# Kernel optimization log

Measured on AMD Instinct MI355X. Metric: run time of the kernel, lower is better.

The kernel has to match this reference:

```python
import jax, jax.numpy as jnp
import numpy as np

N = 50000
E_RAND = 800000
F_IN = 256
F_OUT = 256
ALPHA = 0.2  # LeakyReLU negative slope


def setup_inputs() -> dict:
    key = jax.random.key(0)
    k1, k2, k3, k4 = jax.random.split(key, 4)
    x = jax.random.normal(k1, (N, F_IN), dtype=jnp.float32)
    # random edges + self-loops so every row has at least one edge (avoids div by 0)
    edge_rand = jax.random.randint(k2, (2, E_RAND), 0, N)
    loops = jnp.arange(N)
    edge = jnp.concatenate([edge_rand, jnp.stack([loops, loops])], axis=1)  # [2, 850000]
    W = jax.random.normal(k3, (F_IN, F_OUT), dtype=jnp.float32) * 0.05
    a = jax.random.normal(k4, (2 * F_OUT,), dtype=jnp.float32) * 0.05
    return {"x": x, "edge": edge, "W": W, "a": a}


def reference(x, edge, W, a):
    # x: [N, F_in], edge: [2, E] (row = dst/aggregation index per torch.sparse.mm(a, h))
    n = x.shape[0]
    f_out = W.shape[1]
    h = x @ W  # [N, F_out]
    src, dst = edge[0], edge[1]
    # a @ [h_src; h_dst] decomposes into two per-node dot products (no [E, 2F] concat)
    s = h @ a[:f_out]   # [N]
    t = h @ a[f_out:]   # [N]
    logit = s[src] + t[dst]                                  # [E]
    e = jnp.exp(-jax.nn.leaky_relu(logit, ALPHA))            # [E]
    rowsum = jax.ops.segment_sum(e, src, num_segments=n)     # [N]
    msg = e[:, None] * h[dst]                                # [E, F_out]
    h_prime = jax.ops.segment_sum(msg, src, num_segments=n)  # [N, F_out]
    h_prime = h_prime / rowsum[:, None]
    return jax.nn.relu(h_prime)  # concat=True path
```

## Files before the change

kernel.cpp:

```cpp
#include <hip/hip_runtime.h>
#include <hip/hip_fp16.h>

#define FDIM 256
#define ALPHA 0.2f

typedef _Float16 half8 __attribute__((ext_vector_type(8)));
typedef float floatx4 __attribute__((ext_vector_type(4)));

__global__ __launch_bounds__(256) void prep_hist(const float* __restrict__ W,
                                                 _Float16* __restrict__ wswz,
                                                 const int* __restrict__ edge,
                                                 int* __restrict__ deg, int E) {
  if (blockIdx.x < 32) {
    const int g = blockIdx.x * 256 + threadIdx.x;
    const int kc = g >> 11, L = g & 2047;
    const int n = L >> 3, c = L & 7;
    half8 hv;
#pragma unroll
    for (int j = 0; j < 8; ++j)
      hv[j] = (_Float16)W[(size_t)(kc * 64 + c * 8 + j) * 256 + n];
    *(half8*)(wswz + (size_t)g * 8) = hv;
  } else {
    const int e = (blockIdx.x - 32) * 256 + threadIdx.x;
    if (e < E) atomicAdd(&deg[edge[e]], 1);
  }
}

#define HT_STRIDE 264
__global__ __launch_bounds__(256) void gemm_mfma(
    const float* __restrict__ x, const _Float16* __restrict__ wswz,
    const float* __restrict__ a, _Float16* __restrict__ h,
    float* __restrict__ s, float* __restrict__ t, int M) {
  __shared__ __align__(16) _Float16 smem[64 * HT_STRIDE];
  _Float16* As = smem;
  const int tid = threadIdx.x;
  const int w = tid >> 6, l = tid & 63;
  const int l15 = l & 15, q = l >> 4;
  const int row0 = blockIdx.x * 64;

  floatx4 acc[4][4];
#pragma unroll
  for (int mt = 0; mt < 4; ++mt)
#pragma unroll
    for (int nt = 0; nt < 4; ++nt) acc[mt][nt] = (floatx4){0.f, 0.f, 0.f, 0.f};

  const int id0 = tid, id1 = 256 + tid;
  const int m0 = id0 >> 3, c0 = (id0 & 7) ^ (m0 & 7);
  const int m1 = id1 >> 3, c1 = (id1 & 7) ^ (m1 & 7);
  const int r0 = row0 + m0, r1 = row0 + m1;

  float4 pf[2][2];
  auto loadA = [&](int kc) {
    pf[0][0] = pf[0][1] = pf[1][0] = pf[1][1] = make_float4(0.f, 0.f, 0.f, 0.f);
    if (r0 < M) {
      const float4* p = (const float4*)(x + (size_t)r0 * 256 + kc * 64 + c0 * 8);
      pf[0][0] = p[0];
      pf[0][1] = p[1];
    }
    if (r1 < M) {
      const float4* p = (const float4*)(x + (size_t)r1 * 256 + kc * 64 + c1 * 8);
      pf[1][0] = p[0];
      pf[1][1] = p[1];
    }
  };
  auto storeA = [&]() {
#pragma unroll
    for (int hf = 0; hf < 2; ++hf) {
      half8 hv;
      hv[0] = (_Float16)pf[hf][0].x; hv[1] = (_Float16)pf[hf][0].y;
      hv[2] = (_Float16)pf[hf][0].z; hv[3] = (_Float16)pf[hf][0].w;
      hv[4] = (_Float16)pf[hf][1].x; hv[5] = (_Float16)pf[hf][1].y;
      hv[6] = (_Float16)pf[hf][1].z; hv[7] = (_Float16)pf[hf][1].w;
      *(half8*)(As + (size_t)(hf * 256 + tid) * 8) = hv;
    }
  };

  loadA(0);
  for (int kc = 0; kc < 4; ++kc) {
    storeA();
    half8 bf[2][4];
#pragma unroll
    for (int ks = 0; ks < 2; ++ks) {
      const int c = ks * 4 + q;
#pragma unroll
      for (int nt = 0; nt < 4; ++nt) {
        const int n = w * 64 + nt * 16 + l15;
        bf[ks][nt] = *(const half8*)(wswz + (size_t)(kc * 2048 + n * 8 + c) * 8);
      }
    }
    __syncthreads();
    if (kc < 3) loadA(kc + 1);
#pragma unroll
    for (int ks = 0; ks < 2; ++ks) {
      const int c = ks * 4 + q;
      half8 af[4];
#pragma unroll
      for (int mt = 0; mt < 4; ++mt) {
        const int m = mt * 16 + l15;
        af[mt] = *(const half8*)(As + (size_t)(m * 8 + (c ^ (m & 7))) * 8);
      }
#pragma unroll
      for (int mt = 0; mt < 4; ++mt)
#pragma unroll
        for (int nt = 0; nt < 4; ++nt)
          acc[mt][nt] = __builtin_amdgcn_mfma_f32_16x16x32_f16(
              af[mt], bf[ks][nt], acc[mt][nt], 0, 0, 0);
    }
    __syncthreads();
  }

#pragma unroll
  for (int mt = 0; mt < 4; ++mt)
#pragma unroll
    for (int nt = 0; nt < 4; ++nt)
#pragma unroll
      for (int r = 0; r < 4; ++r)
        smem[(size_t)(mt * 16 + q * 4 + r) * HT_STRIDE + w * 64 + nt * 16 +
             l15] = (_Float16)acc[mt][nt][r];
  __syncthreads();

  const int w8 = tid >> 5;
  const int colh = (tid & 31) * 8;
#pragma unroll
  for (int p = 0; p < 8; ++p) {
    const int rl = p * 8 + w8;
    const int row = row0 + rl;
    if (row < M)
      *(half8*)(h + (size_t)row * 256 + colh) =
          *(const half8*)(smem + (size_t)rl * HT_STRIDE + colh);
  }

  const int r8 = tid >> 2, seg = tid & 3;
  float sp = 0.f, tp = 0.f;
#pragma unroll
  for (int c8 = 0; c8 < 8; ++c8) {
    const int col = seg * 64 + c8 * 8;
    const half8 hv = *(const half8*)(smem + (size_t)r8 * HT_STRIDE + col);
    const float4 a0 = *(const float4*)(a + col);
    const float4 a1 = *(const float4*)(a + col + 4);
    const float4 b0 = *(const float4*)(a + 256 + col);
    const float4 b1 = *(const float4*)(a + 256 + col + 4);
    sp += (float)hv[0] * a0.x + (float)hv[1] * a0.y + (float)hv[2] * a0.z +
          (float)hv[3] * a0.w + (float)hv[4] * a1.x + (float)hv[5] * a1.y +
          (float)hv[6] * a1.z + (float)hv[7] * a1.w;
    tp += (float)hv[0] * b0.x + (float)hv[1] * b0.y + (float)hv[2] * b0.z +
          (float)hv[3] * b0.w + (float)hv[4] * b1.x + (float)hv[5] * b1.y +
          (float)hv[6] * b1.z + (float)hv[7] * b1.w;
  }
  sp += __shfl_xor(sp, 1);
  sp += __shfl_xor(sp, 2);
  tp += __shfl_xor(tp, 1);
  tp += __shfl_xor(tp, 2);
  if (seg == 0 && row0 + r8 < M) {
    s[row0 + r8] = sp;
    t[row0 + r8] = tp;
  }
}

__global__ __launch_bounds__(1024) void scan1(const int* __restrict__ deg,
                                              int* __restrict__ rowstart,
                                              int* __restrict__ bsum, int n) {
  const int tid = threadIdx.x;
  const int i = blockIdx.x * 1024 + tid;
  const int val = (i < n) ? deg[i] : 0;
  const int lane = tid & 63, wv = tid >> 6;
  int v = val;
#pragma unroll
  for (int off = 1; off < 64; off <<= 1) {
    const int o = __shfl_up(v, off);
    if (lane >= off) v += o;
  }
  __shared__ int wsum[16];
  __shared__ int woff[16];
  if (lane == 63) wsum[wv] = v;
  __syncthreads();
  if (tid < 16) {
    int wv2 = wsum[tid];
#pragma unroll
    for (int off = 1; off < 16; off <<= 1) {
      const int o = __shfl_up(wv2, off);
      if (tid >= off) wv2 += o;
    }
    woff[tid] = wv2;
  }
  __syncthreads();
  const int incl = v + (wv ? woff[wv - 1] : 0);
  if (i < n) rowstart[i] = incl - val;
  if (tid == 1023) bsum[blockIdx.x] = woff[15];
}

__global__ __launch_bounds__(64) void scan2(const int* __restrict__ bsum,
                                            int* __restrict__ boff,
                                            int* __restrict__ rowstart, int nb,
                                            int n) {
  const int tid = threadIdx.x;
  int v = (tid < nb) ? bsum[tid] : 0;
#pragma unroll
  for (int off = 1; off < 64; off <<= 1) {
    const int o = __shfl_up(v, off);
    if (tid >= off) v += o;
  }
  if (tid < nb) boff[tid] = v;
  if (tid == nb - 1) rowstart[n] = v;
}

__global__ __launch_bounds__(1024) void scan3(int* __restrict__ rowstart,
                                              int* __restrict__ rsc,
                                              const int* __restrict__ boff,
                                              int n) {
  const int i = blockIdx.x * 1024 + threadIdx.x;
  if (i < n) {
    const int v = rowstart[i] + (blockIdx.x ? boff[blockIdx.x - 1] : 0);
    rowstart[i] = v;
    rsc[i] = v;
  }
}

__global__ void scatter_kernel(const int* __restrict__ edge,
                               int* __restrict__ rsc,
                               const float* __restrict__ s,
                               const float* __restrict__ t,
                               int2* __restrict__ sde, int E) {
  const int e = blockIdx.x * 256 + threadIdx.x;
  if (e < E) {
    const int src = edge[e];
    const int dst = edge[E + e];
    const float logit = s[src] + t[dst];
    const float lr = logit > 0.f ? logit : ALPHA * logit;
    const float ev = __expf(-lr);
    const int pos = atomicAdd(&rsc[src], 1);
    sde[pos] = make_int2(dst, __float_as_int(ev));
  }
}

__global__ __launch_bounds__(256) void agg_kernel(
    const _Float16* __restrict__ h, const int* __restrict__ rowstart,
    const int2* __restrict__ sde, float* __restrict__ out, int n) {
  const int w = threadIdx.x >> 6, l = threadIdx.x & 63;
  const int row = blockIdx.x * 4 + w;
  if (row >= n) return;
  const int start = rowstart[row], end = rowstart[row + 1];
  const int half = l >> 5;
  const int lh = l & 31;
  const size_t fo = (size_t)lh * 8;
  float acc[8] = {};
  float rs = 0.f;
  int j = start;
  for (; j + 8 <= end; j += 8) {
#pragma unroll
    for (int u = 0; u < 4; ++u) {
      const int2 p = sde[j + u * 2 + half];
      const half8 v = *(const half8*)(h + (size_t)p.x * 256 + fo);
      const float e = __int_as_float(p.y);
      rs += e;
#pragma unroll
      for (int k = 0; k < 8; ++k) acc[k] += e * (float)v[k];
    }
  }
  for (; j < end; j += 2) {
    const int idx = j + half;
    const bool valid = idx < end;
    const int2 p = valid ? sde[idx] : make_int2(0, 0);
    const half8 v = *(const half8*)(h + (size_t)p.x * 256 + fo);
    const float e = valid ? __int_as_float(p.y) : 0.f;
    rs += e;
#pragma unroll
    for (int k = 0; k < 8; ++k) acc[k] += e * (float)v[k];
  }
  rs += __shfl_xor(rs, 32);
#pragma unroll
  for (int k = 0; k < 8; ++k) acc[k] += __shfl_xor(acc[k], 32);
  const float inv = 1.f / rs;
  float4 o;
#pragma unroll
  for (int k = 0; k < 4; ++k) {
    const float vv = acc[half * 4 + k] * inv;
    (&o.x)[k] = vv > 0.f ? vv : 0.f;
  }
  *(float4*)(out + (size_t)row * 256 + lh * 8 + half * 4) = o;
}

extern "C" void kernel_launch(void* const* d_in, const int* in_sizes, int n_in,
                              void* d_out, int out_size, void* d_ws,
                              size_t ws_size, hipStream_t stream) {
  const float* x = (const float*)d_in[0];
  const int* edge = (const int*)d_in[1];
  const float* W = (const float*)d_in[2];
  const float* a = (const float*)d_in[3];
  float* out = (float*)d_out;
  const int N = in_sizes[0] / FDIM;
  const int E = in_sizes[1] / 2;
  const int NB = (N + 1023) / 1024;

  _Float16* h = (_Float16*)d_ws;
  _Float16* wswz = h + (size_t)N * FDIM;
  float* s = (float*)(wswz + 8192 * 8);
  float* t = s + N;
  int* deg = (int*)(t + N);
  int* rsc = deg + N;
  int* rowstart = rsc + N;
  int* bsum = rowstart + N + 2;
  int* boff = bsum + 64;
  int2* sde = (int2*)(boff + 64);

  hipMemsetAsync(deg, 0, (size_t)N * sizeof(int), stream);

  prep_hist<<<32 + (E + 255) / 256, 256, 0, stream>>>(W, wswz, edge, deg, E);
  gemm_mfma<<<(N + 63) / 64, 256, 0, stream>>>(x, wswz, a, h, s, t, N);
  scan1<<<NB, 1024, 0, stream>>>(deg, rowstart, bsum, N);
  scan2<<<1, 64, 0, stream>>>(bsum, boff, rowstart, NB, N);
  scan3<<<NB, 1024, 0, stream>>>(rowstart, rsc, boff, N);
  scatter_kernel<<<(E + 255) / 256, 256, 0, stream>>>(edge, rsc, s, t, sde, E);
  agg_kernel<<<(N + 3) / 4, 256, 0, stream>>>(h, rowstart, sde, out, N);
}
```

Baseline: 272.2 us.

## Fuse scan into single-pass decoupled scan and move edge weight compute into aggregation

Result: slower. 328.0 us (+20.5%).

```diff
diff --git a/kernel.cpp b/kernel.cpp
--- a/kernel.cpp
+++ b/kernel.cpp
@@ -157,11 +157,14 @@
   }
 }
 
-__global__ __launch_bounds__(1024) void scan1(const int* __restrict__ deg,
-                                              int* __restrict__ rowstart,
-                                              int* __restrict__ bsum, int n) {
+__global__ __launch_bounds__(1024) void scan_one(const int* __restrict__ deg,
+                                                 int* __restrict__ rowstart,
+                                                 int* __restrict__ rsc,
+                                                 int* __restrict__ flags,
+                                                 int n, int nb) {
   const int tid = threadIdx.x;
-  const int i = blockIdx.x * 1024 + tid;
+  const int b = blockIdx.x;
+  const int i = b * 1024 + tid;
   const int val = (i < n) ? deg[i] : 0;
   const int lane = tid & 63, wv = tid >> 6;
   int v = val;
@@ -172,6 +175,7 @@
   }
   __shared__ int wsum[16];
   __shared__ int woff[16];
+  __shared__ int sbase;
   if (lane == 63) wsum[wv] = v;
   __syncthreads();
   if (tid < 16) {
@@ -185,61 +189,52 @@
   }
   __syncthreads();
   const int incl = v + (wv ? woff[wv - 1] : 0);
-  if (i < n) rowstart[i] = incl - val;
-  if (tid == 1023) bsum[blockIdx.x] = woff[15];
-}
-
-__global__ __launch_bounds__(64) void scan2(const int* __restrict__ bsum,
-                                            int* __restrict__ boff,
-                                            int* __restrict__ rowstart, int nb,
-                                            int n) {
-  const int tid = threadIdx.x;
-  int v = (tid < nb) ? bsum[tid] : 0;
-#pragma unroll
-  for (int off = 1; off < 64; off <<= 1) {
-    const int o = __shfl_up(v, off);
-    if (tid >= off) v += o;
-  }
-  if (tid < nb) boff[tid] = v;
-  if (tid == nb - 1) rowstart[n] = v;
-}
-
-__global__ __launch_bounds__(1024) void scan3(int* __restrict__ rowstart,
-                                              int* __restrict__ rsc,
-                                              const int* __restrict__ boff,
-                                              int n) {
-  const int i = blockIdx.x * 1024 + threadIdx.x;
+  const int aggregate = woff[15];
+  if (tid == 0) {
+    int base = 0;
+    if (b > 0) {
+      int f;
+      do {
+        f = __hip_atomic_load(&flags[b - 1], __ATOMIC_ACQUIRE,
+                              __HIP_MEMORY_SCOPE_AGENT);
+      } while (f == 0);
+      base = f - 1;
+    }
+    __hip_atomic_store(&flags[b], base + aggregate + 1, __ATOMIC_RELEASE,
+                       __HIP_MEMORY_SCOPE_AGENT);
+    sbase = base;
+  }
+  __syncthreads();
+  const int base = sbase;
   if (i < n) {
-    const int v = rowstart[i] + (blockIdx.x ? boff[blockIdx.x - 1] : 0);
-    rowstart[i] = v;
-    rsc[i] = v;
-  }
+    const int ex = base + incl - val;
+    rowstart[i] = ex;
+    rsc[i] = ex;
+  }
+  if (b == nb - 1 && tid == 0) rowstart[n] = base + aggregate;
 }
 
 __global__ void scatter_kernel(const int* __restrict__ edge,
-                               int* __restrict__ rsc,
-                               const float* __restrict__ s,
-                               const float* __restrict__ t,
-                               int2* __restrict__ sde, int E) {
+                               int* __restrict__ rsc, int* __restrict__ sdst,
+                               int E) {
   const int e = blockIdx.x * 256 + threadIdx.x;
   if (e < E) {
     const int src = edge[e];
     const int dst = edge[E + e];
-    const float logit = s[src] + t[dst];
-    const float lr = logit > 0.f ? logit : ALPHA * logit;
-    const float ev = __expf(-lr);
     const int pos = atomicAdd(&rsc[src], 1);
-    sde[pos] = make_int2(dst, __float_as_int(ev));
+    sdst[pos] = dst;
   }
 }
 
 __global__ __launch_bounds__(256) void agg_kernel(
-    const _Float16* __restrict__ h, const int* __restrict__ rowstart,
-    const int2* __restrict__ sde, float* __restrict__ out, int n) {
+    const _Float16* __restrict__ h, const float* __restrict__ s,
+    const float* __restrict__ t, const int* __restrict__ rowstart,
+    const int* __restrict__ sdst, float* __restrict__ out, int n) {
   const int w = threadIdx.x >> 6, l = threadIdx.x & 63;
   const int row = blockIdx.x * 4 + w;
   if (row >= n) return;
   const int start = rowstart[row], end = rowstart[row + 1];
+  const float srow = s[row];
   const int half = l >> 5;
   const int lh = l & 31;
   const size_t fo = (size_t)lh * 8;
@@ -249,9 +244,11 @@
   for (; j + 8 <= end; j += 8) {
 #pragma unroll
     for (int u = 0; u < 4; ++u) {
-      const int2 p = sde[j + u * 2 + half];
-      const half8 v = *(const half8*)(h + (size_t)p.x * 256 + fo);
-      const float e = __int_as_float(p.y);
+      const int d = sdst[j + u * 2 + half];
+      const float logit = srow + t[d];
+      const float lr = logit > 0.f ? logit : ALPHA * logit;
+      const float e = __expf(-lr);
+      const half8 v = *(const half8*)(h + (size_t)d * 256 + fo);
       rs += e;
 #pragma unroll
       for (int k = 0; k < 8; ++k) acc[k] += e * (float)v[k];
@@ -260,9 +257,11 @@
   for (; j < end; j += 2) {
     const int idx = j + half;
     const bool valid = idx < end;
-    const int2 p = valid ? sde[idx] : make_int2(0, 0);
-    const half8 v = *(const half8*)(h + (size_t)p.x * 256 + fo);
-    const float e = valid ? __int_as_float(p.y) : 0.f;
+    const int d = valid ? sdst[idx] : 0;
+    const float logit = srow + t[d];
+    const float lr = logit > 0.f ? logit : ALPHA * logit;
+    const float e = valid ? __expf(-lr) : 0.f;
+    const half8 v = *(const half8*)(h + (size_t)d * 256 + fo);
     rs += e;
 #pragma unroll
     for (int k = 0; k < 8; ++k) acc[k] += e * (float)v[k];
@@ -297,19 +296,16 @@
   float* s = (float*)(wswz + 8192 * 8);
   float* t = s + N;
   int* deg = (int*)(t + N);
-  int* rsc = deg + N;
+  int* flags = deg + N;
+  int* rsc = flags + 64;
   int* rowstart = rsc + N;
-  int* bsum = rowstart + N + 2;
-  int* boff = bsum + 64;
-  int2* sde = (int2*)(boff + 64);
-
-  hipMemsetAsync(deg, 0, (size_t)N * sizeof(int), stream);
+  int* sdst = rowstart + N + 2;
+
+  hipMemsetAsync(deg, 0, (size_t)(N + 64) * sizeof(int), stream);
 
   prep_hist<<<32 + (E + 255) / 256, 256, 0, stream>>>(W, wswz, edge, deg, E);
+  scan_one<<<NB, 1024, 0, stream>>>(deg, rowstart, rsc, flags, N, NB);
+  scatter_kernel<<<(E + 255) / 256, 256, 0, stream>>>(edge, rsc, sdst, E);
   gemm_mfma<<<(N + 63) / 64, 256, 0, stream>>>(x, wswz, a, h, s, t, N);
-  scan1<<<NB, 1024, 0, stream>>>(deg, rowstart, bsum, N);
-  scan2<<<1, 64, 0, stream>>>(bsum, boff, rowstart, NB, N);
-  scan3<<<NB, 1024, 0, stream>>>(rowstart, rsc, boff, N);
-  scatter_kernel<<<(E + 255) / 256, 256, 0, stream>>>(edge, rsc, s, t, sde, E);
-  agg_kernel<<<(N + 3) / 4, 256, 0, stream>>>(h, rowstart, sde, out, N);
-}
+  agg_kernel<<<(N + 3) / 4, 256, 0, stream>>>(h, s, t, rowstart, sdst, out, N);
+}
```
